# Performance work log

Hardware: AMD Instinct MI355X
Metric: run time of the kernel (lower is better)

The kernel has to match this reference:

```python
import jax, jax.numpy as jnp
import numpy as np

N = 100000          # nodes
E = 1600000         # edges
IN_FEATS = 128
OUT_FEATS = 32      # per head
NUM_HEADS = 8
NEG_SLOPE = 0.2     # DGL GATConv default leaky_relu slope


def setup_inputs() -> dict:
    key = jax.random.key(0)
    k_feat, k_src, k_dst, k_w, k_al, k_ar = jax.random.split(key, 6)
    feat = jax.random.normal(k_feat, (N, IN_FEATS), dtype=jnp.float32)
    src = jax.random.randint(k_src, (E,), 0, N, dtype=jnp.int32)
    dst = jax.random.randint(k_dst, (E,), 0, N, dtype=jnp.int32)
    # learned params of GATConv (fc weight, attn vectors, output bias)
    W = jax.random.normal(k_w, (IN_FEATS, NUM_HEADS * OUT_FEATS), dtype=jnp.float32) * 0.05
    attn_l = jax.random.normal(k_al, (NUM_HEADS, OUT_FEATS), dtype=jnp.float32) * 0.05
    attn_r = jax.random.normal(k_ar, (NUM_HEADS, OUT_FEATS), dtype=jnp.float32) * 0.05
    bias = jnp.zeros((NUM_HEADS * OUT_FEATS,), dtype=jnp.float32)
    return {"feat": feat, "src": src, "dst": dst, "W": W,
            "attn_l": attn_l, "attn_r": attn_r, "bias": bias}


def reference(feat, src, dst, W, attn_l, attn_r, bias):
    # Linear projection: [N, H, D]
    ft = (feat @ W).reshape(N, NUM_HEADS, OUT_FEATS)
    # Per-node attention logit halves: [N, H]
    el = jnp.einsum('nhd,hd->nh', ft, attn_l)
    er = jnp.einsum('nhd,hd->nh', ft, attn_r)
    # Per-edge raw score: [E, H]
    e = jax.nn.leaky_relu(el[src] + er[dst], NEG_SLOPE)
    # Edge softmax over incoming edges of each dst node (segment softmax)
    e_max = jax.ops.segment_max(e, dst, num_segments=N)          # [N, H]
    e_exp = jnp.exp(e - e_max[dst])                              # [E, H]
    e_sum = jax.ops.segment_sum(e_exp, dst, num_segments=N)     # [N, H]
    a = e_exp / e_sum[dst]                                       # [E, H]
    # Weighted message aggregation: [N, H, D]
    msg = ft[src] * a[:, :, None]                                # [E, H, D]
    rst = jax.ops.segment_sum(msg, dst, num_segments=N)
    rst = rst + bias.reshape(NUM_HEADS, OUT_FEATS)
    # Head mean (wrapper): [N, D]
    h = rst.mean(axis=1)
    attn = a[:, :, None]                                         # [E, H, 1] as in DGL
    return (h, attn)
```

## Files before the change

### kernel.cpp

```cpp
#include <hip/hip_runtime.h>
#include <hip/hip_bf16.h>

#define NN 100000
#define NE 1600000
#define KF 128
#define CT 256
#define NH 8
#define SL 56
#define GB 1563
#define S_SPLIT 57600
#define SB2 1024
#define AB3 1024
#define EB2 10600

typedef __attribute__((ext_vector_type(8))) short short8;
typedef __attribute__((ext_vector_type(4))) float f32x4;

__device__ __forceinline__ float bf2f(unsigned short u) {
  union { unsigned int i; float f; } x; x.i = ((unsigned int)u) << 16; return x.f;
}
__device__ __forceinline__ unsigned short f2bf(float f) {
  unsigned int b = __float_as_uint(f);
  b += 0x7fffu + ((b >> 16) & 1u);
  return (unsigned short)(b >> 16);
}
__device__ __forceinline__ float lrelu(float e) { return (e > 0.f) ? e : 0.2f * e; }


__device__ __forceinline__ void scatter_range(
    const int* __restrict__ src, const int* __restrict__ dst,
    int* __restrict__ cnt, int* __restrict__ csr,
    int blk, int nblocks, int lo, int hi, int tid)
{
  const int stride = nblocks * 256;
  for (int e = blk * 256 + tid; e < NE; e += stride) {
    int d = dst[e];
    if (d >= lo && d < hi) {
      int sv = src[e];
      int p = atomicAdd(&cnt[d], 1);
      if (p < SL) csr[d * SL + p] = sv;
    }
  }
}

__device__ __forceinline__ void edge_node(
    int n, int lane,
    const int* __restrict__ cnt, const int* __restrict__ csr,
    const float* __restrict__ el, float* __restrict__ ei,
    const unsigned short* __restrict__ ftb, const float* __restrict__ bias,
    float* __restrict__ hout)
{
  int deg = cnt[n];
  if (deg > SL) deg = SL;
  const int beg = n * SL;

  if (deg == 0) {
    if (lane < 8) {
      ei[(size_t)n * 16 + 8 + lane] = 0.f;
      float b0 = 0.f, b1 = 0.f, b2 = 0.f, b3 = 0.f;
#pragma unroll
      for (int hh = 0; hh < NH; hh++) {
        const float* bp = bias + hh * 32 + lane * 4;
        b0 += bp[0]; b1 += bp[1]; b2 += bp[2]; b3 += bp[3];
      }
      float* op = hout + (size_t)n * 32 + lane * 4;
      *(float4*)op = make_float4(b0 * 0.125f, b1 * 0.125f, b2 * 0.125f, b3 * 0.125f);
    }
    return;
  }

  const int h = lane & 7;
  const int q = lane >> 3;
  const float er_v = ei[(size_t)n * 16 + h];
  const int cv = csr[beg + ((lane < SL) ? lane : 0)];
  const int NG = (deg + 7) >> 3;

  float elv[7];
#pragma unroll
  for (int g = 0; g < 7; g++) {
    elv[g] = 0.f;
    if (g < NG) {
      int si = g * 8 + q; si = (si < deg) ? si : (deg - 1);
      int sn = __shfl(cv, si);
      elv[g] = el[(size_t)sn * NH + h];
    }
  }

  float acc0 = 0.f, acc1 = 0.f, acc2 = 0.f, acc3 = 0.f;
  float wsum = 0.f;
  ushort4 ub0[8], ub1[8];

#pragma unroll
  for (int j = 0; j < 8; j++) {
    int si = (j < deg) ? j : (deg - 1);
    int sj = __shfl(cv, si);
    ub0[j] = *(const ushort4*)(ftb + (size_t)sj * CT + lane * 4);
  }
  if (1 < NG) {
#pragma unroll
    for (int j = 0; j < 8; j++) {
      int si = 8 + j; si = (si < deg) ? si : (deg - 1);
      int sj = __shfl(cv, si);
      ub1[j] = *(const ushort4*)(ftb + (size_t)sj * CT + lane * 4);
    }
  }

#pragma unroll
  for (int g = 0; g < 7; g++) {
    if (g < NG) {
      int s = g * 8 + q;
      float e = lrelu(elv[g] + er_v);
      float wv = (s < deg) ? __expf(e) : 0.f;
      wsum += wv;
      float av[8];
#pragma unroll
      for (int j = 0; j < 8; j++) av[j] = __shfl(wv, j * 8 + q);
      if ((g & 1) == 0) {
#pragma unroll
        for (int j = 0; j < 8; j++) {
          acc0 += bf2f(ub0[j].x) * av[j];
          acc1 += bf2f(ub0[j].y) * av[j];
          acc2 += bf2f(ub0[j].z) * av[j];
          acc3 += bf2f(ub0[j].w) * av[j];
        }
        if (g + 2 < NG) {
#pragma unroll
          for (int j = 0; j < 8; j++) {
            int si = (g + 2) * 8 + j; si = (si < deg) ? si : (deg - 1);
            int sj = __shfl(cv, si);
            ub0[j] = *(const ushort4*)(ftb + (size_t)sj * CT + lane * 4);
          }
        }
      } else {
#pragma unroll
        for (int j = 0; j < 8; j++) {
          acc0 += bf2f(ub1[j].x) * av[j];
          acc1 += bf2f(ub1[j].y) * av[j];
          acc2 += bf2f(ub1[j].z) * av[j];
          acc3 += bf2f(ub1[j].w) * av[j];
        }
        if (g + 2 < NG) {
#pragma unroll
          for (int j = 0; j < 8; j++) {
            int si = (g + 2) * 8 + j; si = (si < deg) ? si : (deg - 1);
            int sj = __shfl(cv, si);
            ub1[j] = *(const ushort4*)(ftb + (size_t)sj * CT + lane * 4);
          }
        }
      }
    }
  }

  wsum += __shfl_xor(wsum, 8); wsum += __shfl_xor(wsum, 16); wsum += __shfl_xor(wsum, 32);
  const float inv = 1.f / wsum;
  if (lane < 8) ei[(size_t)n * 16 + 8 + lane] = inv;

  const float invh = __shfl(inv, q);
  acc0 *= invh; acc1 *= invh; acc2 *= invh; acc3 *= invh;

#pragma unroll
  for (int mks = 8; mks <= 32; mks <<= 1) {
    acc0 += __shfl_xor(acc0, mks);
    acc1 += __shfl_xor(acc1, mks);
    acc2 += __shfl_xor(acc2, mks);
    acc3 += __shfl_xor(acc3, mks);
  }
  if (lane < 8) {
    float b0 = 0.f, b1 = 0.f, b2 = 0.f, b3 = 0.f;
#pragma unroll
    for (int hh = 0; hh < NH; hh++) {
      const float* bp = bias + hh * 32 + lane * 4;
      b0 += bp[0]; b1 += bp[1]; b2 += bp[2]; b3 += bp[3];
    }
    float* op = hout + (size_t)n * 32 + lane * 4;
    __builtin_nontemporal_store((acc0 + b0) * 0.125f, op + 0);
    __builtin_nontemporal_store((acc1 + b1) * 0.125f, op + 1);
    __builtin_nontemporal_store((acc2 + b2) * 0.125f, op + 2);
    __builtin_nontemporal_store((acc3 + b3) * 0.125f, op + 3);
  }
}

__device__ __forceinline__ void attn_edge(
    int e, int s, int d,
    const float* __restrict__ el, const float* __restrict__ ei,
    float* __restrict__ attn_out)
{
  const float* lp = el + (size_t)s * NH;
  const float* dp = ei + (size_t)d * 16;
  float4 l0 = *(const float4*)(lp);
  float4 l1 = *(const float4*)(lp + 4);
  float4 r0 = *(const float4*)(dp);
  float4 r1 = *(const float4*)(dp + 4);
  float4 i0 = *(const float4*)(dp + 8);
  float4 i1 = *(const float4*)(dp + 12);
  float* op = attn_out + (size_t)e * NH;
  __builtin_nontemporal_store(__expf(lrelu(l0.x + r0.x)) * i0.x, op + 0);
  __builtin_nontemporal_store(__expf(lrelu(l0.y + r0.y)) * i0.y, op + 1);
  __builtin_nontemporal_store(__expf(lrelu(l0.z + r0.z)) * i0.z, op + 2);
  __builtin_nontemporal_store(__expf(lrelu(l0.w + r0.w)) * i0.w, op + 3);
  __builtin_nontemporal_store(__expf(lrelu(l1.x + r1.x)) * i1.x, op + 4);
  __builtin_nontemporal_store(__expf(lrelu(l1.y + r1.y)) * i1.y, op + 5);
  __builtin_nontemporal_store(__expf(lrelu(l1.z + r1.z)) * i1.z, op + 6);
  __builtin_nontemporal_store(__expf(lrelu(l1.w + r1.w)) * i1.w, op + 7);
}

__global__ void k_wconv(const float* __restrict__ W, unsigned short* __restrict__ Wt) {
  int i = blockIdx.x * 256 + threadIdx.x;
  if (i < KF * CT) {
    int k = i >> 8, c = i & 255;
    Wt[c * KF + k] = f2bf(W[i]);
  }
}

__global__ __launch_bounds__(256) void k_uber(
    const float* __restrict__ feat, const unsigned short* __restrict__ Wt,
    const float* __restrict__ attn_l, const float* __restrict__ attn_r,
    unsigned short* __restrict__ ftb, float* __restrict__ el, float* __restrict__ ei,
    const int* __restrict__ src, const int* __restrict__ dst,
    int* __restrict__ cnt, int* __restrict__ csr)
{
  __shared__ unsigned short fs[64][136];
  const int bid = blockIdx.x;
  const int tid = threadIdx.x;

  if (bid & 1) {
    scatter_range(src, dst, cnt, csr, bid >> 1, GB, 0, S_SPLIT, tid);
    return;
  }

  const int lane = tid & 63, w = tid >> 6;
  const int row0 = (bid >> 1) * 64;

  for (int i = tid; i < 64 * 32; i += 256) {
    int r = i >> 5, c4 = (i & 31) * 4;
    int gr = row0 + r;
    float4 v = make_float4(0.f, 0.f, 0.f, 0.f);
    if (gr < NN) v = *(const float4*)(feat + (size_t)gr * KF + c4);
    *(ushort4*)(&fs[r][c4]) = make_ushort4(f2bf(v.x), f2bf(v.y), f2bf(v.z), f2bf(v.w));
  }

  const int bc = lane & 15;
  const int bk = (lane >> 4) * 8;
  short8 bfrag[4][4];
#pragma unroll
  for (int ks = 0; ks < 4; ks++)
#pragma unroll
    for (int n = 0; n < 4; n++)
      bfrag[ks][n] = *(const short8*)(Wt + (size_t)(w * 64 + n * 16 + bc) * KF + ks * 32 + bk);

  __syncthreads();

  f32x4 acc[4][4];
#pragma unroll
  for (int m = 0; m < 4; m++)
#pragma unroll
    for (int n = 0; n < 4; n++) acc[m][n] = (f32x4){0.f, 0.f, 0.f, 0.f};

#pragma unroll
  for (int ks = 0; ks < 4; ks++) {
    short8 af[4];
#pragma unroll
    for (int m = 0; m < 4; m++)
      af[m] = *(const short8*)(&fs[m * 16 + bc][ks * 32 + bk]);
#pragma unroll
    for (int m = 0; m < 4; m++)
#pragma unroll
      for (int n = 0; n < 4; n++)
        acc[m][n] = __builtin_amdgcn_mfma_f32_16x16x32_bf16(af[m], bfrag[ks][n], acc[m][n], 0, 0, 0);
  }

  const int rbase = (lane >> 4) * 4;

#pragma unroll
  for (int m = 0; m < 4; m++) {
#pragma unroll
    for (int r = 0; r < 4; r++) {
      int gr = row0 + m * 16 + rbase + r;
      if (gr < NN) {
        unsigned short* op = ftb + (size_t)gr * CT + w * 64 + bc;
#pragma unroll
        for (int n = 0; n < 4; n++) op[n * 16] = f2bf(acc[m][n][r]);
      }
    }
  }

  float al[4], ar[4];
#pragma unroll
  for (int n = 0; n < 4; n++) {
    al[n] = attn_l[w * 64 + n * 16 + bc];
    ar[n] = attn_r[w * 64 + n * 16 + bc];
  }
#pragma unroll
  for (int m = 0; m < 4; m++) {
#pragma unroll
    for (int r = 0; r < 4; r++) {
      float pl0 = acc[m][0][r] * al[0] + acc[m][1][r] * al[1];
      float pl1 = acc[m][2][r] * al[2] + acc[m][3][r] * al[3];
      float pr0 = acc[m][0][r] * ar[0] + acc[m][1][r] * ar[1];
      float pr1 = acc[m][2][r] * ar[2] + acc[m][3][r] * ar[3];
#pragma unroll
      for (int d = 1; d < 16; d <<= 1) {
        pl0 += __shfl_xor(pl0, d);
        pl1 += __shfl_xor(pl1, d);
        pr0 += __shfl_xor(pr0, d);
        pr1 += __shfl_xor(pr1, d);
      }
      if (bc == 0) {
        int gr = row0 + m * 16 + rbase + r;
        if (gr < NN) {
          *(float2*)(el + (size_t)gr * NH + 2 * w) = make_float2(pl0, pl1);
          *(float2*)(ei + (size_t)gr * 16 + 2 * w) = make_float2(pr0, pr1);
        }
      }
    }
  }
}

__global__ __launch_bounds__(256) void k_mid(
    const int* __restrict__ src, const int* __restrict__ dst,
    int* __restrict__ cnt, int* __restrict__ csr,
    const float* __restrict__ el, float* __restrict__ ei,
    const unsigned short* __restrict__ ftb, const float* __restrict__ bias,
    float* __restrict__ hout)
{
  const int bid = blockIdx.x;
  if (bid < SB2) {
    scatter_range(src, dst, cnt, csr, bid, SB2, S_SPLIT, NN, threadIdx.x);
    return;
  }
  const int n = (bid - SB2) * 4 + (threadIdx.x >> 6);
  if (n < S_SPLIT)
    edge_node(n, threadIdx.x & 63, cnt, csr, el, ei, ftb, bias, hout);
}

__global__ __launch_bounds__(256) void k_fin(
    const int* __restrict__ src, const int* __restrict__ dst,
    const int* __restrict__ cnt, const int* __restrict__ csr,
    const float* __restrict__ el, float* __restrict__ ei,
    const unsigned short* __restrict__ ftb, const float* __restrict__ bias,
    float* __restrict__ hout, float* __restrict__ attn_out)
{
  const int bid = blockIdx.x;
  if (bid < EB2) {
    const int n = S_SPLIT + bid * 4 + (threadIdx.x >> 6);
    if (n < NN)
      edge_node(n, threadIdx.x & 63, cnt, csr, el, ei, ftb, bias, hout);
    return;
  }
  const int blk = bid - EB2;
  const int stride = AB3 * 256;
  for (int e = blk * 256 + threadIdx.x; e < NE; e += stride) {
    int d = dst[e];
    if (d < S_SPLIT) attn_edge(e, src[e], d, el, ei, attn_out);
  }
}

__global__ __launch_bounds__(256) void k_attn2(
    const int* __restrict__ src, const int* __restrict__ dst,
    const float* __restrict__ el, const float* __restrict__ ei,
    float* __restrict__ attn_out)
{
  int e = blockIdx.x * 256 + threadIdx.x;
  if (e < NE) {
    int d = dst[e];
    if (d >= S_SPLIT) attn_edge(e, src[e], d, el, ei, attn_out);
  }
}

extern "C" void kernel_launch(void* const* d_in, const int* in_sizes, int n_in,
                              void* d_out, int out_size, void* d_ws, size_t ws_size,
                              hipStream_t stream) {
  const float* feat   = (const float*)d_in[0];
  const int*   src    = (const int*)d_in[1];
  const int*   dst    = (const int*)d_in[2];
  const float* W      = (const float*)d_in[3];
  const float* attn_l = (const float*)d_in[4];
  const float* attn_r = (const float*)d_in[5];
  const float* bias   = (const float*)d_in[6];

  char* ws = (char*)d_ws;
  size_t o = 0;
  unsigned short* ftb = (unsigned short*)(ws + o); o += (size_t)NN * CT * 2;
  int* csr            = (int*)(ws + o);            o += (size_t)NN * SL * 4;
  float* el           = (float*)(ws + o);          o += (size_t)NN * NH * 4;
  float* ei           = (float*)(ws + o);          o += (size_t)NN * 16 * 4;
  int* cnt            = (int*)(ws + o);            o += (size_t)NN * 4;
  unsigned short* Wt  = (unsigned short*)(ws + o); o += (size_t)CT * KF * 2;

  float* hout     = (float*)d_out;
  float* attn_out = hout + (size_t)NN * 32;

  hipMemsetAsync(cnt, 0, (size_t)NN * sizeof(int), stream);
  k_wconv<<<(KF * CT + 255) / 256, 256, 0, stream>>>(W, Wt);
  k_uber<<<GB * 2, 256, 0, stream>>>(feat, Wt, attn_l, attn_r, ftb, el, ei, src, dst, cnt, csr);
  k_mid<<<SB2 + S_SPLIT / 4, 256, 0, stream>>>(src, dst, cnt, csr, el, ei, ftb, bias, hout);
  k_fin<<<EB2 + AB3, 256, 0, stream>>>(src, dst, cnt, csr, el, ei, ftb, bias, hout, attn_out);
  k_attn2<<<(NE + 255) / 256, 256, 0, stream>>>(src, dst, el, ei, attn_out);
}
```

Measured before the change: 324.2 us.

## Do full CSR scatter in GEMM kernel once, rebalance edge and attention stages

The CSR build, which was split across two kernels with each pass rereading all edges and filtering by destination range, now runs as a single pass in the odd blocks of the projection kernel. Each thread handles four edges and batches its loads and atomics to expose memory-level parallelism. The later stages are rebalanced: the first node half is aggregated alone, then attention for that half overlaps aggregation of the second half. This cuts redundant edge reads, but it puts all scatter atomics inside the GEMM kernel and leaves the first aggregation kernel with nothing to overlap.

```diff
diff --git a/kernel.cpp b/kernel.cpp
--- a/kernel.cpp
+++ b/kernel.cpp
@@ -8,10 +8,8 @@
 #define NH 8
 #define SL 56
 #define GB 1563
-#define S_SPLIT 57600
-#define SB2 1024
-#define AB3 1024
-#define EB2 10600
+#define S_SPLIT 50000
+#define ATB 1024
 
 typedef __attribute__((ext_vector_type(8))) short short8;
 typedef __attribute__((ext_vector_type(4))) float f32x4;
@@ -26,20 +24,11 @@
 }
 __device__ __forceinline__ float lrelu(float e) { return (e > 0.f) ? e : 0.2f * e; }
 
-
-__device__ __forceinline__ void scatter_range(
-    const int* __restrict__ src, const int* __restrict__ dst,
-    int* __restrict__ cnt, int* __restrict__ csr,
-    int blk, int nblocks, int lo, int hi, int tid)
-{
-  const int stride = nblocks * 256;
-  for (int e = blk * 256 + tid; e < NE; e += stride) {
-    int d = dst[e];
-    if (d >= lo && d < hi) {
-      int sv = src[e];
-      int p = atomicAdd(&cnt[d], 1);
-      if (p < SL) csr[d * SL + p] = sv;
-    }
+__global__ void k_wconv(const float* __restrict__ W, unsigned short* __restrict__ Wt) {
+  int i = blockIdx.x * 256 + threadIdx.x;
+  if (i < KF * CT) {
+    int k = i >> 8, c = i & 255;
+    Wt[c * KF + k] = f2bf(W[i]);
   }
 }
 
@@ -204,14 +193,6 @@
   __builtin_nontemporal_store(__expf(lrelu(l1.w + r1.w)) * i1.w, op + 7);
 }
 
-__global__ void k_wconv(const float* __restrict__ W, unsigned short* __restrict__ Wt) {
-  int i = blockIdx.x * 256 + threadIdx.x;
-  if (i < KF * CT) {
-    int k = i >> 8, c = i & 255;
-    Wt[c * KF + k] = f2bf(W[i]);
-  }
-}
-
 __global__ __launch_bounds__(256) void k_uber(
     const float* __restrict__ feat, const unsigned short* __restrict__ Wt,
     const float* __restrict__ attn_l, const float* __restrict__ attn_r,
@@ -224,7 +205,20 @@
   const int tid = threadIdx.x;
 
   if (bid & 1) {
-    scatter_range(src, dst, cnt, csr, bid >> 1, GB, 0, S_SPLIT, tid);
+    const int base = (bid >> 1) * 1024 + tid;
+    int dv[4], sv[4], p[4];
+#pragma unroll
+    for (int k = 0; k < 4; k++) {
+      int e = base + k * 256;
+      dv[k] = (e < NE) ? dst[e] : -1;
+      sv[k] = (e < NE) ? src[e] : 0;
+    }
+#pragma unroll
+    for (int k = 0; k < 4; k++)
+      if (dv[k] >= 0) p[k] = atomicAdd(&cnt[dv[k]], 1);
+#pragma unroll
+    for (int k = 0; k < 4; k++)
+      if (dv[k] >= 0 && p[k] < SL) csr[dv[k] * SL + p[k]] = sv[k];
     return;
   }
 
@@ -316,24 +310,18 @@
   }
 }
 
-__global__ __launch_bounds__(256) void k_mid(
-    const int* __restrict__ src, const int* __restrict__ dst,
-    int* __restrict__ cnt, int* __restrict__ csr,
+__global__ __launch_bounds__(256) void k_edge1(
+    const int* __restrict__ cnt, const int* __restrict__ csr,
     const float* __restrict__ el, float* __restrict__ ei,
     const unsigned short* __restrict__ ftb, const float* __restrict__ bias,
     float* __restrict__ hout)
 {
-  const int bid = blockIdx.x;
-  if (bid < SB2) {
-    scatter_range(src, dst, cnt, csr, bid, SB2, S_SPLIT, NN, threadIdx.x);
-    return;
-  }
-  const int n = (bid - SB2) * 4 + (threadIdx.x >> 6);
+  const int n = blockIdx.x * 4 + (threadIdx.x >> 6);
   if (n < S_SPLIT)
     edge_node(n, threadIdx.x & 63, cnt, csr, el, ei, ftb, bias, hout);
 }
 
-__global__ __launch_bounds__(256) void k_fin(
+__global__ __launch_bounds__(256) void k_mix(
     const int* __restrict__ src, const int* __restrict__ dst,
     const int* __restrict__ cnt, const int* __restrict__ csr,
     const float* __restrict__ el, float* __restrict__ ei,
@@ -341,18 +329,17 @@
     float* __restrict__ hout, float* __restrict__ attn_out)
 {
   const int bid = blockIdx.x;
-  if (bid < EB2) {
-    const int n = S_SPLIT + bid * 4 + (threadIdx.x >> 6);
-    if (n < NN)
-      edge_node(n, threadIdx.x & 63, cnt, csr, el, ei, ftb, bias, hout);
+  if (bid < ATB) {
+    const int stride = ATB * 256;
+    for (int e = bid * 256 + threadIdx.x; e < NE; e += stride) {
+      int d = dst[e];
+      if (d < S_SPLIT) attn_edge(e, src[e], d, el, ei, attn_out);
+    }
     return;
   }
-  const int blk = bid - EB2;
-  const int stride = AB3 * 256;
-  for (int e = blk * 256 + threadIdx.x; e < NE; e += stride) {
-    int d = dst[e];
-    if (d < S_SPLIT) attn_edge(e, src[e], d, el, ei, attn_out);
-  }
+  const int n = S_SPLIT + (bid - ATB) * 4 + (threadIdx.x >> 6);
+  if (n < NN)
+    edge_node(n, threadIdx.x & 63, cnt, csr, el, ei, ftb, bias, hout);
 }
 
 __global__ __launch_bounds__(256) void k_attn2(
@@ -393,7 +380,7 @@
   hipMemsetAsync(cnt, 0, (size_t)NN * sizeof(int), stream);
   k_wconv<<<(KF * CT + 255) / 256, 256, 0, stream>>>(W, Wt);
   k_uber<<<GB * 2, 256, 0, stream>>>(feat, Wt, attn_l, attn_r, ftb, el, ei, src, dst, cnt, csr);
-  k_mid<<<SB2 + S_SPLIT / 4, 256, 0, stream>>>(src, dst, cnt, csr, el, ei, ftb, bias, hout);
-  k_fin<<<EB2 + AB3, 256, 0, stream>>>(src, dst, cnt, csr, el, ei, ftb, bias, hout, attn_out);
+  k_edge1<<<S_SPLIT / 4, 256, 0, stream>>>(cnt, csr, el, ei, ftb, bias, hout);
+  k_mix<<<ATB + (NN - S_SPLIT + 3) / 4, 256, 0, stream>>>(src, dst, cnt, csr, el, ei, ftb, bias, hout, attn_out);
   k_attn2<<<(NE + 255) / 256, 256, 0, stream>>>(src, dst, el, ei, attn_out);
 }
```

New measurement: 288.7 us. -11.0%, faster.
